# Kernel tuning notes

Measured on AMD Instinct MI355X. Metric: run time of the kernel, lower is better.

The kernel has to match this reference:

```python
import jax, jax.numpy as jnp
import numpy as np

D_MODEL = 1024
D_STATE = 16
D_CONV = 4
EXPAND = 2
D_INNER = EXPAND * D_MODEL           # 2048
DT_RANK = (D_MODEL + 15) // 16       # 64
BATCH = 2
SEQ = 1024


def setup_inputs() -> dict:
    key = jax.random.key(0)
    ks = jax.random.split(key, 8)
    s = 0.02
    x = jax.random.normal(ks[0], (BATCH, SEQ, D_MODEL), jnp.float32)
    in_proj_w = jax.random.normal(ks[1], (2 * D_INNER, D_MODEL), jnp.float32) * s
    conv_w = jax.random.normal(ks[2], (D_INNER, 1, D_CONV), jnp.float32) * s
    conv_b = jnp.zeros((D_INNER,), jnp.float32)
    x_proj_w = jax.random.normal(ks[3], (DT_RANK + 2 * D_STATE, D_INNER), jnp.float32) * s
    dt_proj_w = jax.random.normal(ks[4], (D_INNER, DT_RANK), jnp.float32) * s
    # bias init so softplus(dt) lands in a sane small-dt range
    dt_proj_b = jnp.full((D_INNER,), -4.0, jnp.float32) + 0.1 * jax.random.normal(ks[5], (D_INNER,), jnp.float32)
    # standard S4D-real init: A = -[1..d_state], stored as log
    A_log = jnp.log(jnp.broadcast_to(jnp.arange(1, D_STATE + 1, dtype=jnp.float32), (D_INNER, D_STATE)))
    D_param = jnp.ones((D_INNER,), jnp.float32)
    out_proj_w = jax.random.normal(ks[6], (D_MODEL, D_INNER), jnp.float32) * s
    ln_w = jnp.ones((D_MODEL,), jnp.float32)
    ln_b = jnp.zeros((D_MODEL,), jnp.float32)
    return dict(x=x, in_proj_w=in_proj_w, conv_w=conv_w, conv_b=conv_b,
                x_proj_w=x_proj_w, dt_proj_w=dt_proj_w, dt_proj_b=dt_proj_b,
                A_log=A_log, D_param=D_param, out_proj_w=out_proj_w,
                ln_w=ln_w, ln_b=ln_b)


def _vim_block(x, in_proj_w, conv_w, conv_b, x_proj_w, dt_proj_w, dt_proj_b,
               A_log, D_param, out_proj_w, ln_w, ln_b):
    B, L, Dm = x.shape
    # in_proj (no bias) -> split into conv branch and gate z
    xz = jnp.einsum('bld,ed->ble', x, in_proj_w)          # (B,L,2*d_inner)
    xc, z = jnp.split(xz, 2, axis=-1)
    # causal depthwise conv1d over time
    xc_ncl = jnp.transpose(xc, (0, 2, 1))                  # (B,d_inner,L)
    conv = jax.lax.conv_general_dilated(
        xc_ncl, conv_w, window_strides=(1,), padding=[(D_CONV - 1, 0)],
        dimension_numbers=('NCH', 'OIH', 'NCH'), feature_group_count=D_INNER)
    conv = conv + conv_b[None, :, None]
    u = jax.nn.silu(jnp.transpose(conv, (0, 2, 1)))        # (B,L,d_inner)
    # input-dependent dt, B, C
    x_dbl = jnp.einsum('bld,ed->ble', u, x_proj_w)         # (B,L,dt_rank+2N)
    dt, Bmat, Cmat = jnp.split(x_dbl, [DT_RANK, DT_RANK + D_STATE], axis=-1)
    delta = jax.nn.softplus(jnp.einsum('blr,dr->bld', dt, dt_proj_w) + dt_proj_b)  # (B,L,d_inner)
    A = -jnp.exp(A_log)                                    # (d_inner,N)
    # discretize: ZOH for A, Euler for B (as in mamba selective_scan)
    deltaA = jnp.exp(delta[..., None] * A)                 # (B,L,d_inner,N)
    deltaBu = (delta * u)[..., None] * Bmat[:, :, None, :] # (B,L,d_inner,N)

    def step(h, inp):
        dA_t, dBu_t, C_t = inp                             # (B,d,N),(B,d,N),(B,N)
        h = dA_t * h + dBu_t
        y_t = jnp.einsum('bdn,bn->bd', h, C_t)
        return h, y_t

    h0 = jnp.zeros((B, D_INNER, D_STATE), x.dtype)
    xs = (jnp.moveaxis(deltaA, 1, 0), jnp.moveaxis(deltaBu, 1, 0), jnp.moveaxis(Cmat, 1, 0))
    _, ys = jax.lax.scan(step, h0, xs)                     # ys: (L,B,d_inner)
    y = jnp.moveaxis(ys, 0, 1) + u * D_param               # (B,L,d_inner)
    y = y * jax.nn.silu(z)                                 # gate
    out = jnp.einsum('bld,ed->ble', y, out_proj_w)         # (B,L,D)
    # residual + LayerNorm
    r = x + out
    mu = jnp.mean(r, axis=-1, keepdims=True)
    var = jnp.mean(jnp.square(r - mu), axis=-1, keepdims=True)
    return (r - mu) * jax.lax.rsqrt(var + 1e-5) * ln_w + ln_b


def reference(x, in_proj_w, conv_w, conv_b, x_proj_w, dt_proj_w, dt_proj_b,
              A_log, D_param, out_proj_w, ln_w, ln_b):
    return _vim_block(x, in_proj_w, conv_w, conv_b, x_proj_w, dt_proj_w, dt_proj_b,
                      A_log, D_param, out_proj_w, ln_w, ln_b)
```

## Files before the change

kernel.cpp:

```cpp
#include <hip/hip_runtime.h>
#include <math.h>

#define D_MODEL 1024
#define D_STATE 16
#define D_INNER 2048
#define DT_RANK 64
#define BATCH 2
#define SEQ 1024
#define NTOK (BATCH*SEQ)
#define NC 32
#define TC 32

typedef __attribute__((ext_vector_type(8))) short short8;
typedef __attribute__((ext_vector_type(4))) float f32x4;

__device__ __forceinline__ float siluf(float x){ return x / (1.0f + __expf(-x)); }
__device__ __forceinline__ float softplusf(float x){ return x > 20.f ? x : log1pf(__expf(x)); }

__device__ __forceinline__ unsigned short f2bf(float f){
    unsigned int x = __float_as_uint(f);
    unsigned int r = (x + 0x7FFFu + ((x >> 16) & 1u)) >> 16;
    return (unsigned short)r;
}
__device__ __forceinline__ float bf2f(unsigned short u){
    return __uint_as_float(((unsigned int)u) << 16);
}

__device__ __forceinline__ void gl_lds16(const unsigned short* g, unsigned short* l)
{
    __builtin_amdgcn_global_load_lds(
        (const __attribute__((address_space(1))) unsigned int*)g,
        (__attribute__((address_space(3))) unsigned int*)l, 16, 0, 0);
}

#define CR0 524288
#define CR1 1572864
#define CR2 1622016
#define CR3 1654784
#define CR4 2179072
__global__ __launch_bounds__(256)
void cvt_all(const float* __restrict__ s0, const float* __restrict__ s1,
             const float* __restrict__ s2, const float* __restrict__ s3,
             const float* __restrict__ s4,
             unsigned short* __restrict__ d0, unsigned short* __restrict__ d1,
             unsigned short* __restrict__ d2, unsigned short* __restrict__ d3,
             unsigned short* __restrict__ d4)
{
    int i = blockIdx.x * 256 + threadIdx.x;
    const float* s; unsigned short* dd; int base;
    if      (i < CR0) { s = s0; dd = d0; base = 0;   }
    else if (i < CR1) { s = s1; dd = d1; base = CR0; }
    else if (i < CR2) { s = s2; dd = d2; base = CR1; }
    else if (i < CR3) { s = s3; dd = d3; base = CR2; }
    else              { s = s4; dd = d4; base = CR3; }
    int j = (i - base) * 4;
    float4 v = *reinterpret_cast<const float4*>(&s[j]);
    ushort4 o;
    o.x = f2bf(v.x); o.y = f2bf(v.y); o.z = f2bf(v.z); o.w = f2bf(v.w);
    *reinterpret_cast<ushort4*>(&dd[j]) = o;
}

template<int EPI, int OB>
__global__ __launch_bounds__(256)
void gemm128(const unsigned short* __restrict__ A, int lda,
             const unsigned short* __restrict__ W, int ldw,
             const float* __restrict__ bias,
             void* __restrict__ Cv, int ldc,
             int M, int K)
{
    __shared__ __align__(16) unsigned short As[128 * 32];
    __shared__ __align__(16) unsigned short Ws[128 * 32];
    float* Cf = (float*)Cv;
    unsigned short* Cb = (unsigned short*)Cv;
    const int tid = threadIdx.x;

    const int nwg = gridDim.x * gridDim.y;
    int orig = blockIdx.y * gridDim.x + blockIdx.x;
    const int q = nwg >> 3, r = nwg & 7;
    int xcd = orig & 7, sub = orig >> 3;
    int wg = (xcd < r ? xcd * (q + 1) : r * (q + 1) + (xcd - r) * q) + sub;
    const int m0 = (wg / gridDim.x) * 128;
    const int n0 = (wg % gridDim.x) * 128;

    const size_t kbase = (size_t)blockIdx.z * K;
    Cf += (size_t)blockIdx.z * M * ldc;

    const int wave = tid >> 6, lane = tid & 63;
    const int wr = wave >> 1, wc = wave & 1;
    const int lr = lane & 15, lg = lane >> 4;

    const int gr = lane >> 2;
    const int gc = (lane & 3) * 8;
    const unsigned short* Ab = A + kbase + gc + (size_t)(m0 + wave * 32 + gr) * lda;
    const unsigned short* Wb = W + kbase + gc + (size_t)(n0 + wave * 32 + gr) * ldw;
    unsigned short* lA = &As[(wave * 32) * 32];
    unsigned short* lW = &Ws[(wave * 32) * 32];

    f32x4 acc[4][4];
#pragma unroll
    for (int i = 0; i < 4; i++)
#pragma unroll
        for (int j = 0; j < 4; j++) acc[i][j] = (f32x4)0.f;

    for (int k0 = 0; k0 < K; k0 += 32) {
        gl_lds16(Ab + k0,             lA);
        gl_lds16(Ab + k0 + 16 * lda,  lA + 16 * 32);
        gl_lds16(Wb + k0,             lW);
        gl_lds16(Wb + k0 + 16 * ldw,  lW + 16 * 32);
        __syncthreads();
        short8 af[4], bfr[4];
#pragma unroll
        for (int i = 0; i < 4; i++)
            af[i] = *reinterpret_cast<const short8*>(&As[(wr * 64 + i * 16 + lr) * 32 + lg * 8]);
#pragma unroll
        for (int j = 0; j < 4; j++)
            bfr[j] = *reinterpret_cast<const short8*>(&Ws[(wc * 64 + j * 16 + lr) * 32 + lg * 8]);
#pragma unroll
        for (int i = 0; i < 4; i++)
#pragma unroll
            for (int j = 0; j < 4; j++)
                acc[i][j] = __builtin_amdgcn_mfma_f32_16x16x32_bf16(af[i], bfr[j], acc[i][j], 0, 0, 0);
        __syncthreads();
    }

#pragma unroll
    for (int i = 0; i < 4; i++) {
#pragma unroll
        for (int j = 0; j < 4; j++) {
            int col = n0 + wc * 64 + j * 16 + lr;
            int rbase = m0 + wr * 64 + i * 16 + lg * 4;
#pragma unroll
            for (int q2 = 0; q2 < 4; q2++) {
                float v = acc[i][j][q2];
                if (EPI == 1) v = softplusf(v + bias[col]);
                if (OB) Cb[(size_t)(rbase + q2) * ldc + col] = f2bf(v);
                else    Cf[(size_t)(rbase + q2) * ldc + col] = v;
            }
        }
    }
}

template<int BN>
__global__ __launch_bounds__(256)
void mfma_gemm_sn(const unsigned short* __restrict__ A, int lda,
                  const unsigned short* __restrict__ W, int ldw,
                  float* __restrict__ C, int ldc,
                  int M, int K)
{
    const int LDST = 40;
    __shared__ unsigned short As[128 * LDST];
    __shared__ unsigned short Ws[BN * LDST];
    const int tid = threadIdx.x;
    const int m0 = blockIdx.y * 128;
    const int kbase = blockIdx.z * K;
    C += (size_t)blockIdx.z * M * ldc;

    const int wave = tid >> 6, lane = tid & 63;
    const int wr = wave >> 1, wc = wave & 1;
    const int lr = lane & 15, lg = lane >> 4;
    const int MI = 4, NI = BN / 32;

    f32x4 acc[MI][NI];
#pragma unroll
    for (int i = 0; i < MI; i++)
#pragma unroll
        for (int j = 0; j < NI; j++) acc[i][j] = (f32x4)0.f;

    for (int k0 = 0; k0 < K; k0 += 32) {
        for (int f = tid; f < 128 * 4; f += 256) {
            int r = f >> 2, kq = (f & 3) * 8;
            short8 v = *reinterpret_cast<const short8*>(&A[(size_t)(m0 + r) * lda + kbase + k0 + kq]);
            *reinterpret_cast<short8*>(&As[r * LDST + kq]) = v;
        }
        for (int f = tid; f < BN * 4; f += 256) {
            int r = f >> 2, kq = (f & 3) * 8;
            short8 v = *reinterpret_cast<const short8*>(&W[(size_t)r * ldw + kbase + k0 + kq]);
            *reinterpret_cast<short8*>(&Ws[r * LDST + kq]) = v;
        }
        __syncthreads();
        short8 af[MI], bfr[NI];
#pragma unroll
        for (int i = 0; i < MI; i++)
            af[i] = *reinterpret_cast<const short8*>(&As[(wr * 64 + i * 16 + lr) * LDST + lg * 8]);
#pragma unroll
        for (int j = 0; j < NI; j++)
            bfr[j] = *reinterpret_cast<const short8*>(&Ws[(wc * (BN / 2) + j * 16 + lr) * LDST + lg * 8]);
#pragma unroll
        for (int i = 0; i < MI; i++)
#pragma unroll
            for (int j = 0; j < NI; j++)
                acc[i][j] = __builtin_amdgcn_mfma_f32_16x16x32_bf16(af[i], bfr[j], acc[i][j], 0, 0, 0);
        __syncthreads();
    }

#pragma unroll
    for (int i = 0; i < MI; i++) {
#pragma unroll
        for (int j = 0; j < NI; j++) {
            int col = wc * (BN / 2) + j * 16 + lr;
            int rbase = m0 + wr * 64 + i * 16 + lg * 4;
#pragma unroll
            for (int q = 0; q < 4; q++)
                C[(size_t)(rbase + q) * ldc + col] = acc[i][j][q];
        }
    }
}

__global__ __launch_bounds__(256)
void conv_silu(const unsigned short* __restrict__ xz, const float* __restrict__ cw,
               const float* __restrict__ cb, unsigned short* __restrict__ u)
{
    int idx = blockIdx.x * 256 + threadIdx.x;
    int c = idx & (D_INNER - 1);
    int l = (idx >> 11) & (SEQ - 1);
    int b = idx >> 21;
    float4 w = *reinterpret_cast<const float4*>(&cw[c * 4]);
    float wk[4] = {w.x, w.y, w.z, w.w};
    float acc = cb[c];
    const unsigned short* xp = xz + (size_t)b * SEQ * (2 * D_INNER) + c;
#pragma unroll
    for (int k = 0; k < 4; k++) {
        int lk = l - 3 + k;
        if (lk >= 0) acc = fmaf(wk[k], bf2f(xp[(size_t)lk * (2 * D_INNER)]), acc);
    }
    u[idx] = f2bf(siluf(acc));
}

__global__ __launch_bounds__(256)
void reduce_xproj(const float* __restrict__ part, float* __restrict__ xdbl,
                  unsigned short* __restrict__ dt_bf)
{
    int idx = blockIdx.x * 256 + threadIdx.x;
    float s = 0.f;
#pragma unroll
    for (int z = 0; z < 8; z++) s += part[(size_t)z * NTOK * 96 + idx];
    xdbl[idx] = s;
    int c = idx % 96, m = idx / 96;
    if (c < DT_RANK) dt_bf[m * DT_RANK + c] = f2bf(s);
}

__global__ __launch_bounds__(256)
void scan_phase1(const unsigned short* __restrict__ delta, const unsigned short* __restrict__ u,
                 const float* __restrict__ xdbl,  const float* __restrict__ A_log,
                 float* __restrict__ P, float* __restrict__ Q)
{
    __shared__ float sB[TC][16];
    const int tid = threadIdx.x;
    const int dblk = blockIdx.x & 7;
    const int cc = (blockIdx.x >> 3) & (NC - 1);
    const int b  = blockIdx.x >> 8;
    const int d  = dblk * 256 + tid;
    const int t0 = cc * TC;

    float A[16];
#pragma unroll
    for (int i = 0; i < 4; i++) {
        float4 al = *reinterpret_cast<const float4*>(&A_log[d * 16 + i * 4]);
        A[i*4+0] = -__expf(al.x); A[i*4+1] = -__expf(al.y);
        A[i*4+2] = -__expf(al.z); A[i*4+3] = -__expf(al.w);
    }
    for (int e = tid; e < TC * 16; e += 256) {
        int t = e >> 4, j = e & 15;
        sB[t][j] = xdbl[((size_t)b * SEQ + t0 + t) * 96 + DT_RANK + j];
    }
    __syncthreads();

    float h[16];
#pragma unroll
    for (int n = 0; n < 16; n++) h[n] = 0.f;
    float sum = 0.f;
#pragma unroll 4
    for (int t = 0; t < TC; t++) {
        size_t tok = (size_t)b * SEQ + t0 + t;
        float dv = bf2f(delta[tok * D_INNER + d]);
        float uv = bf2f(u[tok * D_INNER + d]);
        sum += dv;
        float du = dv * uv;
#pragma unroll
        for (int n = 0; n < 16; n++)
            h[n] = fmaf(__expf(dv * A[n]), h[n], du * sB[t][n]);
    }
    size_t off = ((size_t)(cc * BATCH + b) * D_INNER + d) * 16;
#pragma unroll
    for (int i = 0; i < 4; i++) {
        float4 pv = make_float4(__expf(A[i*4+0]*sum), __expf(A[i*4+1]*sum),
                                __expf(A[i*4+2]*sum), __expf(A[i*4+3]*sum));
        *reinterpret_cast<float4*>(&P[off + i*4]) = pv;
        *reinterpret_cast<float4*>(&Q[off + i*4]) =
            make_float4(h[i*4+0], h[i*4+1], h[i*4+2], h[i*4+3]);
    }
}

__global__ __launch_bounds__(256)
void scan_phase2(const float* __restrict__ P, float* __restrict__ Q)
{
    int idx = blockIdx.x * 256 + threadIdx.x;
    int b = idx >> 15, rem = idx & 32767;
    float h = 0.f;
#pragma unroll
    for (int cc = 0; cc < NC; cc++) {
        size_t off = (size_t)(cc * BATCH + b) * (D_INNER * D_STATE) + rem;
        float p = P[off], q = Q[off];
        Q[off] = h;
        h = fmaf(p, h, q);
    }
}

__global__ __launch_bounds__(256)
void scan_phase3(const unsigned short* __restrict__ delta, const unsigned short* __restrict__ u,
                 const unsigned short* __restrict__ xz, const float* __restrict__ xdbl,
                 const float* __restrict__ A_log, const float* __restrict__ Dp,
                 const float* __restrict__ Hin,   unsigned short* __restrict__ yg)
{
    __shared__ float sB[TC][16], sC[TC][16];
    const int tid = threadIdx.x;
    const int dblk = blockIdx.x & 7;
    const int cc = (blockIdx.x >> 3) & (NC - 1);
    const int b  = blockIdx.x >> 8;
    const int d  = dblk * 256 + tid;
    const int t0 = cc * TC;

    float A[16];
#pragma unroll
    for (int i = 0; i < 4; i++) {
        float4 al = *reinterpret_cast<const float4*>(&A_log[d * 16 + i * 4]);
        A[i*4+0] = -__expf(al.x); A[i*4+1] = -__expf(al.y);
        A[i*4+2] = -__expf(al.z); A[i*4+3] = -__expf(al.w);
    }
    const float Dcoef = Dp[d];
    for (int e = tid; e < TC * 16; e += 256) {
        int t = e >> 4, j = e & 15;
        size_t tok = (size_t)b * SEQ + t0 + t;
        sB[t][j] = xdbl[tok * 96 + DT_RANK + j];
        sC[t][j] = xdbl[tok * 96 + DT_RANK + D_STATE + j];
    }
    float h[16];
    {
        size_t off = ((size_t)(cc * BATCH + b) * D_INNER + d) * 16;
#pragma unroll
        for (int i = 0; i < 4; i++) {
            float4 hv = *reinterpret_cast<const float4*>(&Hin[off + i*4]);
            h[i*4+0] = hv.x; h[i*4+1] = hv.y; h[i*4+2] = hv.z; h[i*4+3] = hv.w;
        }
    }
    __syncthreads();

#pragma unroll 4
    for (int t = 0; t < TC; t++) {
        size_t tok = (size_t)b * SEQ + t0 + t;
        float dv = bf2f(delta[tok * D_INNER + d]);
        float uv = bf2f(u[tok * D_INNER + d]);
        float zv = bf2f(xz[tok * (2 * D_INNER) + D_INNER + d]);
        float du = dv * uv;
        float y = 0.f;
#pragma unroll
        for (int n = 0; n < 16; n++) {
            h[n] = fmaf(__expf(dv * A[n]), h[n], du * sB[t][n]);
            y = fmaf(h[n], sC[t][n], y);
        }
        y += uv * Dcoef;
        yg[tok * D_INNER + d] = f2bf(y * siluf(zv));
    }
}

__global__ __launch_bounds__(256)
void ln4_kernel(const float* __restrict__ x, const float* __restrict__ p,
                const float* __restrict__ w, const float* __restrict__ bsc,
                float* __restrict__ out)
{
    __shared__ float red[2][4];
    const int t = blockIdx.x;
    const size_t base = (size_t)t * D_MODEL;
    const size_t S = (size_t)NTOK * D_MODEL;
    const int tid = threadIdx.x;
    float v[4]; float s = 0.f, s2 = 0.f;
#pragma unroll
    for (int i = 0; i < 4; i++) {
        size_t idx = base + tid + i * 256;
        float r = x[idx] + p[idx] + p[S + idx] + p[2 * S + idx] + p[3 * S + idx];
        v[i] = r; s += r; s2 = fmaf(r, r, s2);
    }
#pragma unroll
    for (int off = 32; off >= 1; off >>= 1) {
        s  += __shfl_down(s,  off);
        s2 += __shfl_down(s2, off);
    }
    int lane = tid & 63, wid = tid >> 6;
    if (lane == 0) { red[0][wid] = s; red[1][wid] = s2; }
    __syncthreads();
    float S1 = red[0][0] + red[0][1] + red[0][2] + red[0][3];
    float S2 = red[1][0] + red[1][1] + red[1][2] + red[1][3];
    float mu  = S1 * (1.f / D_MODEL);
    float var = S2 * (1.f / D_MODEL) - mu * mu;
    float rstd = rsqrtf(var + 1e-5f);
#pragma unroll
    for (int i = 0; i < 4; i++) {
        int idx = tid + i * 256;
        out[base + idx] = (v[i] - mu) * rstd * w[idx] + bsc[idx];
    }
}

extern "C" void kernel_launch(void* const* d_in, const int* in_sizes, int n_in,
                              void* d_out, int out_size, void* d_ws, size_t ws_size,
                              hipStream_t stream)
{
    const float* x         = (const float*)d_in[0];
    const float* in_proj_w = (const float*)d_in[1];
    const float* conv_w    = (const float*)d_in[2];
    const float* conv_b    = (const float*)d_in[3];
    const float* x_proj_w  = (const float*)d_in[4];
    const float* dt_proj_w = (const float*)d_in[5];
    const float* dt_proj_b = (const float*)d_in[6];
    const float* A_log     = (const float*)d_in[7];
    const float* D_param   = (const float*)d_in[8];
    const float* out_proj_w= (const float*)d_in[9];
    const float* ln_w      = (const float*)d_in[10];
    const float* ln_b      = (const float*)d_in[11];
    float* out = (float*)d_out;

    unsigned short* xzb = (unsigned short*)d_ws;
    float* xdbl     = (float*)(xzb + (size_t)NTOK * 4096);
    float* partials = xdbl + (size_t)NTOK * 96;
    unsigned short* dlb = (unsigned short*)(partials + (size_t)8 * NTOK * 96);
    unsigned short* ub  = dlb + (size_t)NTOK * D_INNER;
    unsigned short* ygb = ub  + (size_t)NTOK * D_INNER;
    unsigned short* xb  = ygb + (size_t)NTOK * D_INNER;
    unsigned short* wib = xb  + (size_t)NTOK * D_MODEL;
    unsigned short* wxb = wib + (size_t)4096 * 1024;
    unsigned short* wdb = wxb + (size_t)96 * 2048;
    unsigned short* wob = wdb + (size_t)2048 * 64;
    unsigned short* dtb = wob + (size_t)1024 * 2048;
    float* Pbuf = (float*)(dtb + (size_t)NTOK * 64);
    float* Qbuf = Pbuf + (size_t)NC * BATCH * D_INNER * D_STATE;
    float* opart = (float*)d_ws;

    dim3 blk(256);

    cvt_all<<<dim3(CR4 / 256), blk, 0, stream>>>(
        x, in_proj_w, x_proj_w, dt_proj_w, out_proj_w,
        xb, wib, wxb, wdb, wob);

    gemm128<0, 1><<<dim3(4096 / 128, NTOK / 128, 1), blk, 0, stream>>>(
        xb, D_MODEL, wib, D_MODEL, nullptr, xzb, 2 * D_INNER, NTOK, D_MODEL);

    conv_silu<<<dim3((NTOK * D_INNER) / 256), blk, 0, stream>>>(xzb, conv_w, conv_b, ub);

    mfma_gemm_sn<96><<<dim3(1, NTOK / 128, 8), blk, 0, stream>>>(
        ub, D_INNER, wxb, D_INNER, partials, 96, NTOK, 2048 / 8);

    reduce_xproj<<<dim3((NTOK * 96) / 256), blk, 0, stream>>>(partials, xdbl, dtb);

    gemm128<1, 1><<<dim3(D_INNER / 128, NTOK / 128, 1), blk, 0, stream>>>(
        dtb, DT_RANK, wdb, DT_RANK, dt_proj_b, dlb, D_INNER, NTOK, DT_RANK);

    scan_phase1<<<dim3(BATCH * NC * (D_INNER / 256)), blk, 0, stream>>>(
        dlb, ub, xdbl, A_log, Pbuf, Qbuf);
    scan_phase2<<<dim3((BATCH * D_INNER * D_STATE) / 256), blk, 0, stream>>>(Pbuf, Qbuf);
    scan_phase3<<<dim3(BATCH * NC * (D_INNER / 256)), blk, 0, stream>>>(
        dlb, ub, xzb, xdbl, A_log, D_param, Qbuf, ygb);

    gemm128<0, 0><<<dim3(D_MODEL / 128, NTOK / 128, 4), blk, 0, stream>>>(
        ygb, D_INNER, wob, D_INNER, nullptr, opart, D_MODEL, NTOK, D_INNER / 4);

    ln4_kernel<<<dim3(NTOK), blk, 0, stream>>>(x, opart, ln_w, ln_b, out);
}
```

Measured before the change: 185.2 us.

## Double-buffer gemm128 LDS, reuse it for x_proj, store out_proj partials as bf16

The gemm128 kernel now keeps two LDS buffers, so the global-to-LDS loads for the next K-slice are issued while MFMAs run on the current one. A column-validity template parameter lets gemm128 replace the separate mfma_gemm_sn kernel for the 96-column x_proj GEMM. The four split-K out_proj partials are written as bf16 into the reused xz buffer instead of fp32. The LayerNorm kernel is vectorized to read and write float4/ushort4. Storing the partials in bf16 halves that write and read traffic but adds rounding before the residual sum. Loading 128 rows of the 96-row x_proj weight reads past it into neighbouring workspace, and those extra columns are masked at store time.

```diff
diff --git a/kernel.cpp b/kernel.cpp
--- a/kernel.cpp
+++ b/kernel.cpp
@@ -60,7 +60,7 @@
     *reinterpret_cast<ushort4*>(&dd[j]) = o;
 }
 
-template<int EPI, int OB>
+template<int EPI, int OB, int NVALID>
 __global__ __launch_bounds__(256)
 void gemm128(const unsigned short* __restrict__ A, int lda,
              const unsigned short* __restrict__ W, int ldw,
@@ -68,8 +68,8 @@
              void* __restrict__ Cv, int ldc,
              int M, int K)
 {
-    __shared__ __align__(16) unsigned short As[128 * 32];
-    __shared__ __align__(16) unsigned short Ws[128 * 32];
+    __shared__ __align__(16) unsigned short As[2][128 * 32];
+    __shared__ __align__(16) unsigned short Ws[2][128 * 32];
     float* Cf = (float*)Cv;
     unsigned short* Cb = (unsigned short*)Cv;
     const int tid = threadIdx.x;
@@ -83,7 +83,8 @@
     const int n0 = (wg % gridDim.x) * 128;
 
     const size_t kbase = (size_t)blockIdx.z * K;
-    Cf += (size_t)blockIdx.z * M * ldc;
+    const size_t zoff = (size_t)blockIdx.z * M * ldc;
+    Cf += zoff; Cb += zoff;
 
     const int wave = tid >> 6, lane = tid & 63;
     const int wr = wave >> 1, wc = wave & 1;
@@ -93,8 +94,7 @@
     const int gc = (lane & 3) * 8;
     const unsigned short* Ab = A + kbase + gc + (size_t)(m0 + wave * 32 + gr) * lda;
     const unsigned short* Wb = W + kbase + gc + (size_t)(n0 + wave * 32 + gr) * ldw;
-    unsigned short* lA = &As[(wave * 32) * 32];
-    unsigned short* lW = &Ws[(wave * 32) * 32];
+    const int lo = (wave * 32) * 32;
 
     f32x4 acc[4][4];
 #pragma unroll
@@ -102,24 +102,35 @@
 #pragma unroll
         for (int j = 0; j < 4; j++) acc[i][j] = (f32x4)0.f;
 
-    for (int k0 = 0; k0 < K; k0 += 32) {
-        gl_lds16(Ab + k0,             lA);
-        gl_lds16(Ab + k0 + 16 * lda,  lA + 16 * 32);
-        gl_lds16(Wb + k0,             lW);
-        gl_lds16(Wb + k0 + 16 * ldw,  lW + 16 * 32);
-        __syncthreads();
+    auto STAGE = [&](int buf, int kk) {
+        gl_lds16(Ab + kk,            &As[buf][lo]);
+        gl_lds16(Ab + kk + 16 * lda, &As[buf][lo + 16 * 32]);
+        gl_lds16(Wb + kk,            &Ws[buf][lo]);
+        gl_lds16(Wb + kk + 16 * ldw, &Ws[buf][lo + 16 * 32]);
+    };
+    auto COMPUTE = [&](int buf) {
         short8 af[4], bfr[4];
 #pragma unroll
         for (int i = 0; i < 4; i++)
-            af[i] = *reinterpret_cast<const short8*>(&As[(wr * 64 + i * 16 + lr) * 32 + lg * 8]);
+            af[i] = *reinterpret_cast<const short8*>(&As[buf][(wr * 64 + i * 16 + lr) * 32 + lg * 8]);
 #pragma unroll
         for (int j = 0; j < 4; j++)
-            bfr[j] = *reinterpret_cast<const short8*>(&Ws[(wc * 64 + j * 16 + lr) * 32 + lg * 8]);
+            bfr[j] = *reinterpret_cast<const short8*>(&Ws[buf][(wc * 64 + j * 16 + lr) * 32 + lg * 8]);
 #pragma unroll
         for (int i = 0; i < 4; i++)
 #pragma unroll
             for (int j = 0; j < 4; j++)
                 acc[i][j] = __builtin_amdgcn_mfma_f32_16x16x32_bf16(af[i], bfr[j], acc[i][j], 0, 0, 0);
+    };
+
+    STAGE(0, 0);
+    __syncthreads();
+    for (int k0 = 0; k0 < K; k0 += 64) {
+        if (k0 + 32 < K) STAGE(1, k0 + 32);
+        COMPUTE(0);
+        __syncthreads();
+        if (k0 + 64 < K) STAGE(0, k0 + 64);
+        COMPUTE(1);
         __syncthreads();
     }
 
@@ -128,6 +139,7 @@
 #pragma unroll
         for (int j = 0; j < 4; j++) {
             int col = n0 + wc * 64 + j * 16 + lr;
+            if (NVALID > 0 && col >= NVALID) continue;
             int rbase = m0 + wr * 64 + i * 16 + lg * 4;
 #pragma unroll
             for (int q2 = 0; q2 < 4; q2++) {
@@ -136,72 +148,6 @@
                 if (OB) Cb[(size_t)(rbase + q2) * ldc + col] = f2bf(v);
                 else    Cf[(size_t)(rbase + q2) * ldc + col] = v;
             }
-        }
-    }
-}
-
-template<int BN>
-__global__ __launch_bounds__(256)
-void mfma_gemm_sn(const unsigned short* __restrict__ A, int lda,
-                  const unsigned short* __restrict__ W, int ldw,
-                  float* __restrict__ C, int ldc,
-                  int M, int K)
-{
-    const int LDST = 40;
-    __shared__ unsigned short As[128 * LDST];
-    __shared__ unsigned short Ws[BN * LDST];
-    const int tid = threadIdx.x;
-    const int m0 = blockIdx.y * 128;
-    const int kbase = blockIdx.z * K;
-    C += (size_t)blockIdx.z * M * ldc;
-
-    const int wave = tid >> 6, lane = tid & 63;
-    const int wr = wave >> 1, wc = wave & 1;
-    const int lr = lane & 15, lg = lane >> 4;
-    const int MI = 4, NI = BN / 32;
-
-    f32x4 acc[MI][NI];
-#pragma unroll
-    for (int i = 0; i < MI; i++)
-#pragma unroll
-        for (int j = 0; j < NI; j++) acc[i][j] = (f32x4)0.f;
-
-    for (int k0 = 0; k0 < K; k0 += 32) {
-        for (int f = tid; f < 128 * 4; f += 256) {
-            int r = f >> 2, kq = (f & 3) * 8;
-            short8 v = *reinterpret_cast<const short8*>(&A[(size_t)(m0 + r) * lda + kbase + k0 + kq]);
-            *reinterpret_cast<short8*>(&As[r * LDST + kq]) = v;
-        }
-        for (int f = tid; f < BN * 4; f += 256) {
-            int r = f >> 2, kq = (f & 3) * 8;
-            short8 v = *reinterpret_cast<const short8*>(&W[(size_t)r * ldw + kbase + k0 + kq]);
-            *reinterpret_cast<short8*>(&Ws[r * LDST + kq]) = v;
-        }
-        __syncthreads();
-        short8 af[MI], bfr[NI];
-#pragma unroll
-        for (int i = 0; i < MI; i++)
-            af[i] = *reinterpret_cast<const short8*>(&As[(wr * 64 + i * 16 + lr) * LDST + lg * 8]);
-#pragma unroll
-        for (int j = 0; j < NI; j++)
-            bfr[j] = *reinterpret_cast<const short8*>(&Ws[(wc * (BN / 2) + j * 16 + lr) * LDST + lg * 8]);
-#pragma unroll
-        for (int i = 0; i < MI; i++)
-#pragma unroll
-            for (int j = 0; j < NI; j++)
-                acc[i][j] = __builtin_amdgcn_mfma_f32_16x16x32_bf16(af[i], bfr[j], acc[i][j], 0, 0, 0);
-        __syncthreads();
-    }
-
-#pragma unroll
-    for (int i = 0; i < MI; i++) {
-#pragma unroll
-        for (int j = 0; j < NI; j++) {
-            int col = wc * (BN / 2) + j * 16 + lr;
-            int rbase = m0 + wr * 64 + i * 16 + lg * 4;
-#pragma unroll
-            for (int q = 0; q < 4; q++)
-                C[(size_t)(rbase + q) * ldc + col] = acc[i][j][q];
         }
     }
 }
@@ -364,7 +310,7 @@
 }
 
 __global__ __launch_bounds__(256)
-void ln4_kernel(const float* __restrict__ x, const float* __restrict__ p,
+void ln4_kernel(const float* __restrict__ x, const unsigned short* __restrict__ p,
                 const float* __restrict__ w, const float* __restrict__ bsc,
                 float* __restrict__ out)
 {
@@ -373,13 +319,20 @@
     const size_t base = (size_t)t * D_MODEL;
     const size_t S = (size_t)NTOK * D_MODEL;
     const int tid = threadIdx.x;
-    float v[4]; float s = 0.f, s2 = 0.f;
-#pragma unroll
-    for (int i = 0; i < 4; i++) {
-        size_t idx = base + tid + i * 256;
-        float r = x[idx] + p[idx] + p[S + idx] + p[2 * S + idx] + p[3 * S + idx];
-        v[i] = r; s += r; s2 = fmaf(r, r, s2);
-    }
+    const int c0 = tid * 4;
+    float4 xv = *reinterpret_cast<const float4*>(&x[base + c0]);
+    ushort4 p0 = *reinterpret_cast<const ushort4*>(&p[base + c0]);
+    ushort4 p1 = *reinterpret_cast<const ushort4*>(&p[S + base + c0]);
+    ushort4 p2 = *reinterpret_cast<const ushort4*>(&p[2 * S + base + c0]);
+    ushort4 p3 = *reinterpret_cast<const ushort4*>(&p[3 * S + base + c0]);
+    float v[4];
+    v[0] = xv.x + bf2f(p0.x) + bf2f(p1.x) + bf2f(p2.x) + bf2f(p3.x);
+    v[1] = xv.y + bf2f(p0.y) + bf2f(p1.y) + bf2f(p2.y) + bf2f(p3.y);
+    v[2] = xv.z + bf2f(p0.z) + bf2f(p1.z) + bf2f(p2.z) + bf2f(p3.z);
+    v[3] = xv.w + bf2f(p0.w) + bf2f(p1.w) + bf2f(p2.w) + bf2f(p3.w);
+    float s = 0.f, s2 = 0.f;
+#pragma unroll
+    for (int i = 0; i < 4; i++) { s += v[i]; s2 = fmaf(v[i], v[i], s2); }
 #pragma unroll
     for (int off = 32; off >= 1; off >>= 1) {
         s  += __shfl_down(s,  off);
@@ -393,11 +346,14 @@
     float mu  = S1 * (1.f / D_MODEL);
     float var = S2 * (1.f / D_MODEL) - mu * mu;
     float rstd = rsqrtf(var + 1e-5f);
-#pragma unroll
-    for (int i = 0; i < 4; i++) {
-        int idx = tid + i * 256;
-        out[base + idx] = (v[i] - mu) * rstd * w[idx] + bsc[idx];
-    }
+    float4 wv = *reinterpret_cast<const float4*>(&w[c0]);
+    float4 bv = *reinterpret_cast<const float4*>(&bsc[c0]);
+    float4 ov;
+    ov.x = (v[0] - mu) * rstd * wv.x + bv.x;
+    ov.y = (v[1] - mu) * rstd * wv.y + bv.y;
+    ov.z = (v[2] - mu) * rstd * wv.z + bv.z;
+    ov.w = (v[3] - mu) * rstd * wv.w + bv.w;
+    *reinterpret_cast<float4*>(&out[base + c0]) = ov;
 }
 
 extern "C" void kernel_launch(void* const* d_in, const int* in_sizes, int n_in,
@@ -432,7 +388,7 @@
     unsigned short* dtb = wob + (size_t)1024 * 2048;
     float* Pbuf = (float*)(dtb + (size_t)NTOK * 64);
     float* Qbuf = Pbuf + (size_t)NC * BATCH * D_INNER * D_STATE;
-    float* opart = (float*)d_ws;
+    unsigned short* opart = xzb;
 
     dim3 blk(256);
 
@@ -440,17 +396,17 @@
         x, in_proj_w, x_proj_w, dt_proj_w, out_proj_w,
         xb, wib, wxb, wdb, wob);
 
-    gemm128<0, 1><<<dim3(4096 / 128, NTOK / 128, 1), blk, 0, stream>>>(
+    gemm128<0, 1, 0><<<dim3(4096 / 128, NTOK / 128, 1), blk, 0, stream>>>(
         xb, D_MODEL, wib, D_MODEL, nullptr, xzb, 2 * D_INNER, NTOK, D_MODEL);
 
     conv_silu<<<dim3((NTOK * D_INNER) / 256), blk, 0, stream>>>(xzb, conv_w, conv_b, ub);
 
-    mfma_gemm_sn<96><<<dim3(1, NTOK / 128, 8), blk, 0, stream>>>(
-        ub, D_INNER, wxb, D_INNER, partials, 96, NTOK, 2048 / 8);
+    gemm128<0, 0, 96><<<dim3(1, NTOK / 128, 8), blk, 0, stream>>>(
+        ub, D_INNER, wxb, D_INNER, nullptr, partials, 96, NTOK, 2048 / 8);
 
     reduce_xproj<<<dim3((NTOK * 96) / 256), blk, 0, stream>>>(partials, xdbl, dtb);
 
-    gemm128<1, 1><<<dim3(D_INNER / 128, NTOK / 128, 1), blk, 0, stream>>>(
+    gemm128<1, 1, 0><<<dim3(D_INNER / 128, NTOK / 128, 1), blk, 0, stream>>>(
         dtb, DT_RANK, wdb, DT_RANK, dt_proj_b, dlb, D_INNER, NTOK, DT_RANK);
 
     scan_phase1<<<dim3(BATCH * NC * (D_INNER / 256)), blk, 0, stream>>>(
@@ -459,7 +415,7 @@
     scan_phase3<<<dim3(BATCH * NC * (D_INNER / 256)), blk, 0, stream>>>(
         dlb, ub, xzb, xdbl, A_log, D_param, Qbuf, ygb);
 
-    gemm128<0, 0><<<dim3(D_MODEL / 128, NTOK / 128, 4), blk, 0, stream>>>(
+    gemm128<0, 1, 0><<<dim3(D_MODEL / 128, NTOK / 128, 4), blk, 0, stream>>>(
         ygb, D_INNER, wob, D_INNER, nullptr, opart, D_MODEL, NTOK, D_INNER / 4);
 
     ln4_kernel<<<dim3(NTOK), blk, 0, stream>>>(x, opart, ln_w, ln_b, out);
```

New measurement: 173.1 us. -6.6%, faster.
